# Kernel optimization log

Hardware: AMD Instinct MI355X
Metric: run time of the kernel (lower is better)

The kernel has to match this reference:

```python
import jax, jax.numpy as jnp
import numpy as np
from functools import partial

M = 48          # state dim m (= n in this module)
N = 48          # obs dim n == m
B = 32          # batch of independent trajectories
T = 128         # time steps (lax.scan)
HQ = M * M      # GRU_Q hidden
HSIG = M * M    # GRU_Sigma hidden
HS = N * N      # GRU_S hidden
D_SIG_IN = HQ + M          # GRU_Sigma input
D_S_IN = N * N + 2 * N     # GRU_S input
FC2_IN = HS + HSIG
FC2_HID = FC2_IN
FC2_OUT = N * N


def _lin(k, dout, din):
    kw, kb = jax.random.split(k)
    s = 1.0 / np.sqrt(din)
    W = jax.random.uniform(kw, (dout, din), jnp.float32, -s, s)
    b = jax.random.uniform(kb, (dout,), jnp.float32, -s, s)
    return W, b


def _gru_params(k, din, dh):
    k1, k2, k3, k4 = jax.random.split(k, 4)
    s = 1.0 / np.sqrt(dh)
    Wi = jax.random.uniform(k1, (3 * dh, din), jnp.float32, -s, s)
    Wh = jax.random.uniform(k2, (3 * dh, dh), jnp.float32, -s, s)
    bi = jax.random.uniform(k3, (3 * dh,), jnp.float32, -s, s)
    bh = jax.random.uniform(k4, (3 * dh,), jnp.float32, -s, s)
    return Wi, Wh, bi, bh


def setup_inputs() -> dict:
    key = jax.random.key(0)
    ks = list(jax.random.split(key, 24))
    it = iter(ks)
    inp = {}
    inp['y_seq'] = jax.random.normal(next(it), (T, B, N), jnp.float32)
    inp['x0'] = jax.random.normal(next(it), (B, M), jnp.float32)
    inp['hQ0'] = jax.random.normal(next(it), (B, HQ), jnp.float32)
    inp['hSig0'] = jax.random.normal(next(it), (B, HSIG), jnp.float32)
    inp['hS0'] = jax.random.normal(next(it), (B, HS), jnp.float32)
    # system matrices (f_function surrogate F, observation H)
    inp['F'] = jax.random.normal(next(it), (M, M), jnp.float32) / np.sqrt(M)
    inp['H'] = jax.random.normal(next(it), (N, M), jnp.float32) / np.sqrt(M)
    # GRUs
    inp['WiQ'], inp['WhQ'], inp['biQ'], inp['bhQ'] = _gru_params(next(it), M, HQ)
    inp['WiSig'], inp['WhSig'], inp['biSig'], inp['bhSig'] = _gru_params(next(it), D_SIG_IN, HSIG)
    inp['WiS'], inp['WhS'], inp['biS'], inp['bhS'] = _gru_params(next(it), D_S_IN, HS)
    # FC blocks
    inp['W1'], inp['b1'] = _lin(next(it), N * N, HSIG)
    inp['W2a'], inp['b2a'] = _lin(next(it), FC2_HID, FC2_IN)
    inp['W2b'], inp['b2b'] = _lin(next(it), FC2_OUT, FC2_HID)
    inp['W3'], inp['b3'] = _lin(next(it), M * M, HS + FC2_OUT)
    inp['W4'], inp['b4'] = _lin(next(it), HSIG, HSIG + M * M)
    inp['W5'], inp['b5'] = _lin(next(it), M, M)
    inp['W6'], inp['b6'] = _lin(next(it), M, M)
    inp['W7'], inp['b7'] = _lin(next(it), 2 * N, 2 * N)
    return inp


def _gru_cell(x, h, Wi, Wh, bi, bh):
    # PyTorch GRU cell: r,z,n gate order
    gi = x @ Wi.T + bi
    gh = h @ Wh.T + bh
    ir, iz, inn = jnp.split(gi, 3, axis=-1)
    hr, hz, hn = jnp.split(gh, 3, axis=-1)
    r = jax.nn.sigmoid(ir + hr)
    z = jax.nn.sigmoid(iz + hz)
    ng = jnp.tanh(inn + r * hn)
    return (1.0 - z) * ng + z * h


def _l2norm(x):
    # torch F.normalize(p=2, eps=1e-12)
    return x / jnp.maximum(jnp.linalg.norm(x, axis=-1, keepdims=True), 1e-12)


def reference(y_seq, x0, hQ0, hSig0, hS0, F, H,
              WiQ, WhQ, biQ, bhQ, WiSig, WhSig, biSig, bhSig,
              WiS, WhS, biS, bhS,
              W1, b1, W2a, b2a, W2b, b2b, W3, b3, W4, b4,
              W5, b5, W6, b6, W7, b7):
    relu = jax.nn.relu

    def step(carry, y):
        x_post, x_post_prev, x_prior_prev, y_prev, hQ, hSig, hS = carry
        # step_prior (Lorenz branch): m1x_prior = F(x) @ x ; m1y = H @ m1x_prior
        x_prior = x_post @ F.T                       # [B, M]
        m1y = x_prior @ H.T                          # [B, N]
        # step_KGain_est: four normalized difference features
        obs_diff = _l2norm(y - y_prev)
        obs_innov = _l2norm(y - m1y)
        fw_evol = _l2norm(x_post - x_post_prev)
        fw_upd = _l2norm(x_post - x_prior_prev)
        # KGain_step
        o5 = relu(fw_evol @ W5.T + b5)
        hQ_n = _gru_cell(o5, hQ, WiQ, WhQ, biQ, bhQ)
        o6 = relu(fw_upd @ W6.T + b6)
        hSig_n = _gru_cell(jnp.concatenate([hQ_n, o6], -1), hSig, WiSig, WhSig, biSig, bhSig)
        o1 = relu(hSig_n @ W1.T + b1)
        o7 = relu(jnp.concatenate([obs_diff, obs_innov], -1) @ W7.T + b7)
        hS_n = _gru_cell(jnp.concatenate([o1, o7], -1), hS, WiS, WhS, biS, bhS)
        o2 = relu(jnp.concatenate([hSig_n, hS_n], -1) @ W2a.T + b2a) @ W2b.T + b2b
        o3 = relu(jnp.concatenate([hS_n, o2], -1) @ W3.T + b3)
        o4 = relu(jnp.concatenate([hSig_n, o3], -1) @ W4.T + b4)
        # self.h_Sigma = out_FC4 (GRU_Sigma state overwritten)
        KG = o2.reshape(-1, M, M)                    # KGain, d == m == n
        dy = y - m1y
        x_new = x_prior + jnp.einsum('bij,bj->bi', KG, dy)
        return (x_new, x_post, x_prior, y, hQ_n, o4, hS_n), x_new

    y_prev0 = x0 @ H.T
    carry0 = (x0, x0, x0, y_prev0, hQ0, hSig0, hS0)
    _, x_out = jax.lax.scan(step, carry0, y_seq)     # [T, B, M]
    return x_out
```

## Files before the change

### kernel.cpp

```cpp
#include <hip/hip_runtime.h>


typedef unsigned short u16;
typedef unsigned int u32;
typedef unsigned long long u64;
typedef __attribute__((ext_vector_type(8))) short short8;
typedef __attribute__((ext_vector_type(4))) float f32x4;

#define NBLK 288
#define NLEAF 8
#define LEAFSZ (NBLK / NLEAF)

__device__ __forceinline__ u16 f2bf(float f) {
  union { float f; u32 u; } v; v.f = f;
  u32 r = v.u + 0x7fffu + ((v.u >> 16) & 1u);
  return (u16)(r >> 16);
}

__device__ __forceinline__ float gload_f(const float* p) {
  return __hip_atomic_load(p, __ATOMIC_RELAXED, __HIP_MEMORY_SCOPE_AGENT);
}
__device__ __forceinline__ void gstore_f(float* p, float v) {
  __hip_atomic_store(p, v, __ATOMIC_RELAXED, __HIP_MEMORY_SCOPE_AGENT);
}
__device__ __forceinline__ void gstore_bf(u16* p, u16 v) {
  asm volatile("global_store_short %0, %1, off sc0 sc1"
               :: "v"(p), "v"((u32)v) : "memory");
}
__device__ __forceinline__ short8 gload_frag(const u16* p) {
  u64 lo = __hip_atomic_load((const u64*)p,       __ATOMIC_RELAXED, __HIP_MEMORY_SCOPE_AGENT);
  u64 hi = __hip_atomic_load((const u64*)(p + 4), __ATOMIC_RELAXED, __HIP_MEMORY_SCOPE_AGENT);
  union { u64 q[2]; short8 v; } u; u.q[0] = lo; u.q[1] = hi; return u.v;
}

struct PJob { const float* src; u16* dst; int rows, cols; };
struct PJobs { PJob j[3]; };

__global__ void __launch_bounds__(256) pre_cvt(PJobs jobs) {
  PJob jb = jobs.j[blockIdx.y];
  int r = blockIdx.x;
  if (r >= jb.rows) return;
  const float* s = jb.src + (long)r * jb.cols;
  u16* d = jb.dst + (long)r * jb.cols;
  for (int c = threadIdx.x; c < jb.cols; c += blockDim.x) d[c] = f2bf(s[c]);
}

__global__ void __launch_bounds__(256) sw_cvt(const float* src, u16* dst,
    int cols_in, int col_off, int cols_take, int nkt, int u_row0, int u_dst0) {
  int ul = blockIdx.x;
  int u_row = u_row0 + ul;
  long dstbase = (long)(u_dst0 + ul) * nkt * 512;
  for (int i = threadIdx.x; i < nkt * 64; i += blockDim.x) {
    int kt = i >> 6, l = i & 63;
    int r = u_row * 16 + (l & 15);
    int c = kt * 32 + ((l >> 4) << 3);
    const float* s = src + (long)r * cols_in + col_off + c;
    u16 o[8];
#pragma unroll
    for (int j = 0; j < 8; ++j)
      o[j] = (c + j < cols_take) ? f2bf(s[j]) : (u16)0;
    *(ulonglong2*)(dst + dstbase + (long)kt * 512 + l * 8) = *(ulonglong2*)o;
  }
}

__global__ void __launch_bounds__(256) flat_cp(const u16* src, u16* dst, long n8) {
  long i = (long)blockIdx.x * blockDim.x + threadIdx.x;
  long stride = (long)gridDim.x * blockDim.x;
  for (; i < n8; i += stride)
    ((ulonglong2*)dst)[i] = ((const ulonglong2*)src)[i];
}

struct KParams {
  const float *y_seq, *x0, *hQ0, *hSig0, *hS0, *F, *H;
  const float *biQ, *bhQ, *biSig, *bhSig, *biS, *bhS;
  const float *b1, *b2a, *b2b, *b3, *b4, *W5, *b5, *W6, *b6, *W7, *b7;
  const u16 *WiQp, *WhQp, *WiSigH, *WiSigO, *WhSigp, *WiSp, *WhSp;
  const u16 *W1p, *W2ap, *W2bp, *W3p, *W4p;
  u16 *hQbf, *hSigN, *hSigC, *hSbf, *o1, *o2a, *o2, *o3, *o6, *o7;
  float *ghSig, *ghS, *hQf, *hSigCf, *hSf, *o2f, *xprior, *dy;
  float *out;
  u32 *bar;
};

__device__ __forceinline__ void gridbar(u32* bar) {
  __syncthreads();
  if (threadIdx.x == 0) {
    u32* leaf = bar + (blockIdx.x & (NLEAF - 1)) * 32;
    u32* root = bar + 256;
    u32* gen  = bar + 288;
    u32 g = __hip_atomic_load(gen, __ATOMIC_RELAXED, __HIP_MEMORY_SCOPE_AGENT);
    bool released = false;
    u32 a = __hip_atomic_fetch_add(leaf, 1u, __ATOMIC_RELAXED, __HIP_MEMORY_SCOPE_AGENT);
    if (a == LEAFSZ - 1) {
      __hip_atomic_store(leaf, 0u, __ATOMIC_RELAXED, __HIP_MEMORY_SCOPE_AGENT);
      asm volatile("s_waitcnt vmcnt(0)" ::: "memory");
      u32 r = __hip_atomic_fetch_add(root, 1u, __ATOMIC_RELAXED, __HIP_MEMORY_SCOPE_AGENT);
      if (r == NLEAF - 1) {
        __hip_atomic_store(root, 0u, __ATOMIC_RELAXED, __HIP_MEMORY_SCOPE_AGENT);
        asm volatile("s_waitcnt vmcnt(0)" ::: "memory");
        __hip_atomic_store(gen, g + 1u, __ATOMIC_RELAXED, __HIP_MEMORY_SCOPE_AGENT);
        released = true;
      }
    }
    if (!released) {
      while (__hip_atomic_load(gen, __ATOMIC_RELAXED, __HIP_MEMORY_SCOPE_AGENT) == g) {
        __builtin_amdgcn_s_sleep(2);
      }
    }
  }
  __syncthreads();
}

template<int NCH, bool AG>
__device__ __forceinline__ void mm6(f32x4& acc, const u16* __restrict__ wp,
                                    const u16* __restrict__ ap) {
  short8 aw[2][6], ab[2][6];
#pragma unroll
  for (int i = 0; i < 6; ++i) {
    aw[0][i] = *(const short8*)(wp + (long)i * 512);
    ab[0][i] = AG ? gload_frag(ap + i * 32) : *(const short8*)(ap + i * 32);
  }
#pragma unroll
  for (int ch = 0; ch < NCH; ++ch) {
    const int cur = ch & 1;
    if (ch + 1 < NCH) {
#pragma unroll
      for (int i = 0; i < 6; ++i) {
        aw[cur ^ 1][i] = *(const short8*)(wp + (long)((ch + 1) * 6 + i) * 512);
        ab[cur ^ 1][i] = AG ? gload_frag(ap + ((ch + 1) * 6 + i) * 32)
                            : *(const short8*)(ap + ((ch + 1) * 6 + i) * 32);
      }
    }
#pragma unroll
    for (int i = 0; i < 6; ++i)
      acc = __builtin_amdgcn_mfma_f32_16x16x32_bf16(aw[cur][i], ab[cur][i], acc, 0, 0, 0);
  }
}

__device__ __forceinline__ const u16* wfrag(const u16* Wf, long unit, int NKT, int kt) {
  return Wf + ((long)unit * NKT + kt) * 512;
}

template<bool AG>
__device__ __forceinline__ void mm72(f32x4& acc, const u16* Wf, long unit, int NKT,
                                     int wkt0, const u16* act ,
                                     int astride, int wave, int lane) {
  int k0 = wave * 18;
  const u16* wp = wfrag(Wf, unit, NKT, wkt0 + k0) + lane * 8;
  const u16* ap = act + (long)(lane & 15) * astride + ((lane >> 4) << 3) + k0 * 32;
  mm6<3, AG>(acc, wp, ap);
}

template<bool AG>
__device__ __forceinline__ void mm144(f32x4& acc, const u16* Wf, long unit, int NKT,
                                      const u16* act, int astride, int wave, int lane) {
  int k0 = wave * 36;
  const u16* wp = wfrag(Wf, unit, NKT, k0) + lane * 8;
  const u16* ap = act + (long)(lane & 15) * astride + ((lane >> 4) << 3) + k0 * 32;
  mm6<6, AG>(acc, wp, ap);
}

template<bool AG>
__device__ __forceinline__ void mm_small(f32x4& acc, const u16* Wf, long unit, int NKT,
                                         const u16* act, int astride, int n,
                                         int wave, int lane) {
  if (wave < n) {
    const u16* wp = wfrag(Wf, unit, NKT, wave) + lane * 8;
    const u16* ap = act + (long)(lane & 15) * astride + ((lane >> 4) << 3) + wave * 32;
    short8 a = *(const short8*)wp;
    short8 b = AG ? gload_frag(ap) : *(const short8*)ap;
    acc = __builtin_amdgcn_mfma_f32_16x16x32_bf16(a, b, acc, 0, 0, 0);
  }
}

__device__ __forceinline__ void block_reduce(float* red, const f32x4* acc, int na,
                                             int wave, int lane, float* out) {
  for (int a = 0; a < na; ++a)
    for (int r = 0; r < 4; ++r)
      red[((wave * 4 + a) * 4 + r) * 64 + lane] = acc[a][r];
  __syncthreads();
  for (int a = 0; a < na; ++a) {
    float s = 0.f;
    for (int w = 0; w < 4; ++w) s += red[((w * 4 + a) * 4 + wave) * 64 + lane];
    out[a] = s;
  }
}

__device__ __forceinline__ void fc_unit(float* red, const u16* W, int NKT, int ctl, int hfl,
    const u16* a0, int s0stride, const u16* a1, int s1stride,
    const float* bias, bool do_relu, u16* outbf, float* outf, bool coh_outf,
    int ostride, int wave, int lane) {
  f32x4 acc = {};
  mm72<true>(acc, W, ctl, NKT, 0, a0 + (long)hfl * 16 * s0stride, s0stride, wave, lane);
  if (a1) mm72<true>(acc, W, ctl, NKT, 72, a1 + (long)hfl * 16 * s1stride, s1stride, wave, lane);
  float v;
  block_reduce(red, &acc, 1, wave, lane, &v);
  int c = ctl * 16 + ((lane >> 4) << 2) + wave;
  int b = hfl * 16 + (lane & 15);
  v += bias[c];
  if (do_relu) v = fmaxf(v, 0.f);
  gstore_bf(outbf + (long)b * ostride + c, f2bf(v));
  if (outf) {
    if (coh_outf) gstore_f(outf + (long)b * ostride + c, v);
    else          outf[(long)b * ostride + c] = v;
  }
  __syncthreads();
}

__device__ __forceinline__ void fc144_unit(float* red, const u16* W, int ctl, int hfl,
    const u16* a0, int s0stride, const float* bias, u16* outbf, float* outf, int ostride,
    int wave, int lane) {
  f32x4 acc = {};
  mm144<true>(acc, W, ctl, 144, a0 + (long)hfl * 16 * s0stride, s0stride, wave, lane);
  float v;
  block_reduce(red, &acc, 1, wave, lane, &v);
  int c = ctl * 16 + ((lane >> 4) << 2) + wave;
  int b = hfl * 16 + (lane & 15);
  v += bias[c];
  gstore_bf(outbf + (long)b * ostride + c, f2bf(v));
  if (outf) gstore_f(outf + (long)b * ostride + c, v);
  __syncthreads();
}

__device__ __forceinline__ void gh_unit(float* red, const u16* Wh, const u16* actbf,
                                        const float* bh, float* ghout,
                                        int ctl, int hfl, int wave, int lane) {
  f32x4 acc[3] = {};
  const u16* ah = actbf + (long)hfl * 16 * 2304;
  for (int g = 0; g < 3; ++g)
    mm72<true>(acc[g], Wh, g * 144 + ctl, 72, 0, ah, 2304, wave, lane);
  float v[3];
  block_reduce(red, acc, 3, wave, lane, v);
  int c = ctl * 16 + ((lane >> 4) << 2) + wave;
  int b = hfl * 16 + (lane & 15);
  for (int g = 0; g < 3; ++g)
    ghout[((long)b * 3 + g) * 2304 + c] = v[g] + bh[g * 2304 + c];
  __syncthreads();
}

__device__ __forceinline__ void gru_gi_unit(float* red,
    const u16* WiMain, int NKTm, const u16* a0, int s0s,
    const u16* WiTail, int NKTt, int tailUnitMul, int wkt0t,
    const u16* a1, int s1s, int ntail,
    const float* bi, const float* gh, const float* hold,
    u16* hbf, float* hf32, int ctl, int hfl, int wave, int lane) {
  f32x4 acc[3] = {};
  const u16* ah = a0 + (long)hfl * 16 * s0s;
  const u16* at = a1 + (long)hfl * 16 * s1s;
  for (int g = 0; g < 3; ++g) {
    mm72<true>(acc[g], WiMain, g * 144 + ctl, NKTm, 0, ah, s0s, wave, lane);
    if (ntail == 0) continue;
    if (tailUnitMul) {
      if (wave < ntail) {
        const u16* wp = wfrag(WiMain, g * 144 + ctl, NKTm, wkt0t + wave) + lane * 8;
        short8 a = *(const short8*)wp;
        short8 b = gload_frag(at + (long)(lane & 15) * s1s + ((lane >> 4) << 3) + wave * 32);
        acc[g] = __builtin_amdgcn_mfma_f32_16x16x32_bf16(a, b, acc[g], 0, 0, 0);
      }
    } else {
      mm_small<true>(acc[g], WiTail, g * 144 + ctl, NKTt, at, s1s, ntail, wave, lane);
    }
  }
  float v[3];
  block_reduce(red, acc, 3, wave, lane, v);
  int c = ctl * 16 + ((lane >> 4) << 2) + wave;
  int b = hfl * 16 + (lane & 15);
  float gr = gh[((long)b * 3 + 0) * 2304 + c];
  float gz = gh[((long)b * 3 + 1) * 2304 + c];
  float gn = gh[((long)b * 3 + 2) * 2304 + c];
  float r  = 1.f / (1.f + expf(-(v[0] + bi[c] + gr)));
  float z  = 1.f / (1.f + expf(-(v[1] + bi[2304 + c] + gz)));
  float nn = tanhf(v[2] + bi[4608 + c] + r * gn);
  float h  = (1.f - z) * nn + z * hold[(long)b * 2304 + c];
  gstore_bf(hbf + (long)b * 2304 + c, f2bf(h));
  if (hf32) hf32[(long)b * 2304 + c] = h;
  __syncthreads();
}

__global__ void __launch_bounds__(256, 2) knet_main(KParams p) {
  const int tid  = threadIdx.x;
  const int blk  = blockIdx.x;
  const int lane = tid & 63;
  const int wave = tid >> 6;
  const int ctb  = blk >> 1;
  const int hfb  = blk & 1;

  __shared__ __align__(16) float red[4096];
  __shared__ __align__(16) float sA[1536];
  __shared__ __align__(16) float sB[1536];
  __shared__ __align__(16) float sC[1536];
  __shared__ __align__(16) u16 sO5[2048];
  __shared__ float sN1[32], sN2[32], sN3[32];

  for (int t = 0; t < 128; ++t) {
    const float* y      = p.y_seq + t * 1536;
    const float* xpost  = (t >= 1) ? (p.out + (t - 1) * 1536) : p.x0;
    const float* xpost2 = (t >= 2) ? (p.out + (t - 2) * 1536) : p.x0;
    const u16* hQbf_r = p.hQbf + (t & 1) * (32 * 2304);
    u16* hQbf_w       = p.hQbf + ((t + 1) & 1) * (32 * 2304);
    const float* hQf_r   = (t == 0) ? p.hQ0   : p.hQf;
    const float* hSigf_r = (t == 0) ? p.hSig0 : p.hSigCf;
    const float* hSf_r   = (t == 0) ? p.hS0   : p.hSf;
    float* xpr_w         = p.xprior + (t & 1) * 1536;
    const float* xprprev = p.xprior + ((t + 1) & 1) * 1536;

    if (blk == 0) {
      if (t >= 1) {
        const float* yp = p.y_seq + (t - 1) * 1536;
        for (int i = tid; i < 1536; i += 256) sA[i] = y[i] - yp[i];
      } else {
        for (int i = tid; i < 1536; i += 256) {
          int b = i / 48, j = i - b * 48;
          float s = 0.f;
          for (int k = 0; k < 48; ++k) s += p.x0[b * 48 + k] * p.H[j * 48 + k];
          sA[i] = y[i] - s;
        }
      }
      for (int i = tid; i < 1536; i += 256) {
        int b = i / 48, j = i - b * 48;
        float s = 0.f;
        for (int k = 0; k < 48; ++k) s += gload_f(&xpost[b * 48 + k]) * p.F[j * 48 + k];
        sB[i] = s;
        gstore_f(&xpr_w[i], s);
      }
      __syncthreads();
      for (int i = tid; i < 1536; i += 256) {
        int b = i / 48, j = i - b * 48;
        float s = 0.f;
        for (int k = 0; k < 48; ++k) s += sB[b * 48 + k] * p.H[j * 48 + k];
        s = y[i] - s;
        sC[i] = s;
        gstore_f(&p.dy[i], s);
      }
      __syncthreads();
      if (tid < 32) {
        float s = 0.f;
        for (int k = 0; k < 48; ++k) { float d = sA[tid * 48 + k]; s += d * d; }
        sN1[tid] = 1.f / fmaxf(sqrtf(s), 1e-12f);
      } else if (tid < 64) {
        int b = tid - 32; float s = 0.f;
        for (int k = 0; k < 48; ++k) { float d = sC[b * 48 + k]; s += d * d; }
        sN2[b] = 1.f / fmaxf(sqrtf(s), 1e-12f);
      }
      __syncthreads();
      {
        const float* xpp = (t == 0) ? p.x0 : xprprev;
        for (int i = tid; i < 1536; i += 256)
          sB[i] = gload_f(&xpost[i]) - gload_f(&xpp[i]);
      }
      __syncthreads();
      if (tid < 32) {
        float s = 0.f;
        for (int k = 0; k < 48; ++k) { float d = sB[tid * 48 + k]; s += d * d; }
        sN3[tid] = 1.f / fmaxf(sqrtf(s), 1e-12f);
      }
      __syncthreads();
      for (int i = tid; i < 2048; i += 256) {
        int b = i >> 6, c = i & 63;
        float v = 0.f;
        if (c < 48) {
          v = p.b6[c]; float nb = sN3[b];
          for (int k = 0; k < 48; ++k) v += sB[b * 48 + k] * nb * p.W6[c * 48 + k];
          v = fmaxf(v, 0.f);
        }
        gstore_bf(&p.o6[i], f2bf(v));
      }
      for (int i = tid; i < 3072; i += 256) {
        int b = i / 96, c = i - b * 96;
        float v = p.b7[c];
        float n1 = sN1[b], n2 = sN2[b];
        for (int k = 0; k < 48; ++k) v += sA[b * 48 + k] * n1 * p.W7[c * 96 + k];
        for (int k = 0; k < 48; ++k) v += sC[b * 48 + k] * n2 * p.W7[c * 96 + 48 + k];
        gstore_bf(&p.o7[i], f2bf(fmaxf(v, 0.f)));
      }
      __syncthreads();
    }

    {
      const int rowbase = hfb * 16;
      for (int i = tid; i < 768; i += 256) {
        int r = i / 48, k = i - r * 48;
        int b = rowbase + r;
        sA[i] = gload_f(&xpost[b * 48 + k]) - gload_f(&xpost2[b * 48 + k]);
      }
      __syncthreads();
      if (tid < 16) {
        float s = 0.f;
        for (int k = 0; k < 48; ++k) { float d = sA[tid * 48 + k]; s += d * d; }
        sN1[tid] = 1.f / fmaxf(sqrtf(s), 1e-12f);
      }
      __syncthreads();
      for (int i = tid; i < 1024; i += 256) {
        int r = i >> 6, c = i & 63;
        float v = 0.f;
        if (c < 48) {
          v = p.b5[c]; float nb = sN1[r];
          for (int k = 0; k < 48; ++k) v += sA[r * 48 + k] * nb * p.W5[c * 48 + k];
          v = fmaxf(v, 0.f);
        }
        sO5[i] = f2bf(v);
      }
      __syncthreads();
    }

    {
      f32x4 acc[4] = {};
      const u16* actH  = hQbf_r + (long)hfb * 16 * 2304;
      const u16* actO5 = (const u16*)sO5;
      for (int g = 0; g < 2; ++g) {
        mm_small<false>(acc[g], p.WiQp, g * 144 + ctb, 2, actO5, 64, 2, wave, lane);
        mm72<true>(acc[g], p.WhQp, g * 144 + ctb, 72, 0, actH, 2304, wave, lane);
      }
      mm_small<false>(acc[2], p.WiQp, 2 * 144 + ctb, 2, actO5, 64, 2, wave, lane);
      mm72<true>(acc[3], p.WhQp, 2 * 144 + ctb, 72, 0, actH, 2304, wave, lane);
      float v[4];
      block_reduce(red, acc, 4, wave, lane, v);
      int c = ctb * 16 + ((lane >> 4) << 2) + wave;
      int b = hfb * 16 + (lane & 15);
      float r  = 1.f / (1.f + expf(-(v[0] + p.biQ[c] + p.bhQ[c])));
      float z  = 1.f / (1.f + expf(-(v[1] + p.biQ[2304 + c] + p.bhQ[2304 + c])));
      float nn = tanhf(v[2] + p.biQ[4608 + c] + r * (v[3] + p.bhQ[4608 + c]));
      float h  = (1.f - z) * nn + z * hQf_r[(long)b * 2304 + c];
      p.hQf[(long)b * 2304 + c] = h;
      gstore_bf(hQbf_w + (long)b * 2304 + c, f2bf(h));
      __syncthreads();
    }
    gh_unit(red, p.WhSigp, p.hSigC, p.bhSig, p.ghSig, ctb, hfb, wave, lane);
    gh_unit(red, p.WhSp,   p.hSbf,  p.bhS,   p.ghS,   ctb, hfb, wave, lane);
    gridbar(p.bar);

    gru_gi_unit(red,
                p.WiSigH, 72, hQbf_w, 2304,
                p.WiSigO, 2, 0, 0, p.o6, 64, 2,
                p.biSig, p.ghSig, hSigf_r,
                p.hSigN, nullptr, ctb, hfb, wave, lane);
    gridbar(p.bar);

    fc_unit(red, p.W1p, 72, ctb, hfb,
            p.hSigN, 2304, nullptr, 0,
            p.b1, true, p.o1, nullptr, false, 2304, wave, lane);
    gridbar(p.bar);

    gru_gi_unit(red,
                p.WiSp, 75, p.o1, 2304,
                nullptr, 0, 1, 72, p.o7, 96, 3,
                p.biS, p.ghS, hSf_r,
                p.hSbf, p.hSf, ctb, hfb, wave, lane);
    gridbar(p.bar);

    for (int uu = blk; uu < 576; uu += NBLK) {
      int ctl = uu >> 1, hfl = uu & 1;
      fc_unit(red, p.W2ap, 144, ctl, hfl,
              p.hSigN, 2304, p.hSbf, 2304,
              p.b2a, true, p.o2a, nullptr, false, 4608, wave, lane);
    }
    gridbar(p.bar);

    fc144_unit(red, p.W2bp, ctb, hfb,
               p.o2a, 4608, p.b2b, p.o2, p.o2f, 2304, wave, lane);
    gridbar(p.bar);

    fc_unit(red, p.W3p, 144, ctb, hfb,
            p.hSbf, 2304, p.o2, 2304,
            p.b3, true, p.o3, nullptr, false, 2304, wave, lane);
    if (blk < 32) {
      const int b = blk;
      for (int ii = tid; ii < 48; ii += 256) {
        float s = gload_f(&xpr_w[b * 48 + ii]);
        const float* o2row = p.o2f + (long)b * 2304 + ii * 48;
        const float* dyrow = p.dy + b * 48;
        for (int j = 0; j < 48; ++j) s += gload_f(&o2row[j]) * gload_f(&dyrow[j]);
        gstore_f(&p.out[t * 1536 + b * 48 + ii], s);
      }
    }
    gridbar(p.bar);

    fc_unit(red, p.W4p, 144, ctb, hfb,
            p.hSigN, 2304, p.o3, 2304,
            p.b4, true, p.hSigC, p.hSigCf, false ,
            2304, wave, lane);
    gridbar(p.bar);
  }
}

extern "C" void kernel_launch(void* const* d_in, const int* in_sizes, int n_in,
                              void* d_out, int out_size, void* d_ws, size_t ws_size,
                              hipStream_t stream) {
  if (n_in < 35) return;
  if (in_sizes[0] != 128 * 32 * 48) return;
  if (in_sizes[7] != 6912 * 48) return;
  if (in_sizes[11] != 6912 * 2352) return;
  if (in_sizes[15] != 6912 * 2400) return;
  if (in_sizes[21] != 4608 * 4608) return;
  if (in_sizes[33] != 96 * 96) return;
  if (out_size != 128 * 32 * 48) return;

  float* in[35];
  for (int i = 0; i < 35; ++i) in[i] = (float*)d_in[i];

  char* base = (char*)d_ws;
  size_t used = 0;
  auto alloc = [&](size_t bytes) -> char* {
    char* r = base + used;
    used += (bytes + 255) & ~(size_t)255;
    return r;
  };
  u32* bar      = (u32*)alloc(2048);
  u16* temp     = (u16*)alloc(2304ll * 4608 * 2);
  u16* WiQp     = (u16*)alloc(432ll * 2 * 512 * 2);
  u16* WiSigO   = (u16*)alloc(432ll * 2 * 512 * 2);
  u16* hQbf     = (u16*)alloc(2ll * 32 * 2304 * 2);
  u16* hSigN    = (u16*)alloc(32ll * 2304 * 2);
  u16* hSigC    = (u16*)alloc(32ll * 2304 * 2);
  u16* hSbf     = (u16*)alloc(32ll * 2304 * 2);
  u16* o1b      = (u16*)alloc(32ll * 2304 * 2);
  u16* o2ab     = (u16*)alloc(32ll * 4608 * 2);
  u16* o2b      = (u16*)alloc(32ll * 2304 * 2);
  u16* o3b      = (u16*)alloc(32ll * 2304 * 2);
  u16* o6b      = (u16*)alloc(32ll * 64 * 2);
  u16* o7b      = (u16*)alloc(32ll * 96 * 2);
  float* ghSig  = (float*)alloc(32ll * 6912 * 4);
  float* ghS    = (float*)alloc(32ll * 6912 * 4);
  float* hQf    = (float*)alloc(32ll * 2304 * 4);
  float* hSigCf = (float*)alloc(32ll * 2304 * 4);
  float* hSf    = (float*)alloc(32ll * 2304 * 4);
  float* o2f    = (float*)alloc(32ll * 2304 * 4);
  float* xprior = (float*)alloc(2ll * 1536 * 4);
  float* dy     = (float*)alloc(1536ll * 4);
  if (used > ws_size) return;

  hipMemsetAsync(bar, 0, 2048, stream);

  PJobs pj;
  pj.j[0] = { in[2], hQbf,  32, 2304 };
  pj.j[1] = { in[3], hSigC, 32, 2304 };
  pj.j[2] = { in[4], hSbf,  32, 2304 };
  pre_cvt<<<dim3(32, 3), dim3(256), 0, stream>>>(pj);

  sw_cvt<<<dim3(432), dim3(256), 0, stream>>>(in[7],  WiQp,   48,   0,    48, 2, 0, 0);
  sw_cvt<<<dim3(432), dim3(256), 0, stream>>>(in[11], WiSigO, 2352, 2304, 48, 2, 0, 0);

  struct IP { float* buf; int rows, ci, take, nkt; };
  const IP ips[10] = {
    { in[8],  6912, 2304, 2304, 72 },
    { in[11], 6912, 2352, 2304, 72 },
    { in[12], 6912, 2304, 2304, 72 },
    { in[15], 6912, 2400, 2400, 75 },
    { in[16], 6912, 2304, 2304, 72 },
    { in[19], 2304, 2304, 2304, 72 },
    { in[21], 4608, 4608, 4608, 144 },
    { in[23], 2304, 4608, 4608, 144 },
    { in[25], 2304, 4608, 4608, 144 },
    { in[27], 2304, 4608, 4608, 144 },
  };
  for (int m = 0; m < 10; ++m) {
    int U = ips[m].rows / 16, Uh = U / 2;
    sw_cvt<<<dim3(Uh), dim3(256), 0, stream>>>(ips[m].buf, temp,
        ips[m].ci, 0, ips[m].take, ips[m].nkt, 0, 0);
    sw_cvt<<<dim3(Uh), dim3(256), 0, stream>>>(ips[m].buf, (u16*)ips[m].buf,
        ips[m].ci, 0, ips[m].take, ips[m].nkt, Uh, Uh);
    long n8 = (long)Uh * ips[m].nkt * 64;
    flat_cp<<<dim3(2048), dim3(256), 0, stream>>>(temp, (u16*)ips[m].buf, n8);
  }

  KParams kp;
  kp.y_seq = in[0]; kp.x0 = in[1]; kp.hQ0 = in[2]; kp.hSig0 = in[3]; kp.hS0 = in[4];
  kp.F = in[5]; kp.H = in[6];
  kp.biQ = in[9]; kp.bhQ = in[10];
  kp.biSig = in[13]; kp.bhSig = in[14];
  kp.biS = in[17]; kp.bhS = in[18];
  kp.b1 = in[20]; kp.b2a = in[22]; kp.b2b = in[24]; kp.b3 = in[26]; kp.b4 = in[28];
  kp.W5 = in[29]; kp.b5 = in[30]; kp.W6 = in[31]; kp.b6 = in[32]; kp.W7 = in[33]; kp.b7 = in[34];
  kp.WiQp = WiQp;
  kp.WhQp = (const u16*)in[8];
  kp.WiSigH = (const u16*)in[11];
  kp.WiSigO = WiSigO;
  kp.WhSigp = (const u16*)in[12];
  kp.WiSp = (const u16*)in[15];
  kp.WhSp = (const u16*)in[16];
  kp.W1p = (const u16*)in[19];
  kp.W2ap = (const u16*)in[21];
  kp.W2bp = (const u16*)in[23];
  kp.W3p = (const u16*)in[25];
  kp.W4p = (const u16*)in[27];
  kp.hQbf = hQbf; kp.hSigN = hSigN; kp.hSigC = hSigC; kp.hSbf = hSbf;
  kp.o1 = o1b; kp.o2a = o2ab; kp.o2 = o2b; kp.o3 = o3b; kp.o6 = o6b; kp.o7 = o7b;
  kp.ghSig = ghSig; kp.ghS = ghS; kp.hQf = hQf; kp.hSigCf = hSigCf; kp.hSf = hSf;
  kp.o2f = o2f; kp.xprior = xprior; kp.dy = dy;
  kp.out = (float*)d_out;
  kp.bar = bar;

  knet_main<<<dim3(NBLK), dim3(256), 0, stream>>>(kp);
}
```

Before: 66.48 ms.

## Share activation fragments across gate matrices in multi-output MFMA loops

Adds a mm_multi helper that loads each activation fragment once and reuses it across 2 or 3 weight slices (GRU gates, or the two halves of W2a). The GRU gh, gi and Q gate computations and the FC2a layer now use it instead of separate mm72 calls per gate. FC2a now handles two output tiles per block in one unit rather than looping over 576 units. This cuts redundant coherent global activation loads and adds independent MFMA chains, at the cost of higher register pressure from larger double-buffered fragment arrays.

Measured after the change: 76.47 ms. 1.15x slower.

```diff
diff --git a/kernel.cpp b/kernel.cpp
--- a/kernel.cpp
+++ b/kernel.cpp
@@ -111,6 +111,64 @@
   __syncthreads();
 }
 
+__device__ __forceinline__ const u16* wfrag(const u16* Wf, long unit, int NKT, int kt) {
+  return Wf + ((long)unit * NKT + kt) * 512;
+}
+
+template<int NS, int CHK, int NCH, bool AG>
+__device__ __forceinline__ void mm_multi(f32x4* acc, const u16* __restrict__ wp0,
+                                         long gs, const u16* __restrict__ ap) {
+  short8 aw[2][NS][CHK];
+  short8 ab[2][CHK];
+#pragma unroll
+  for (int i = 0; i < CHK; ++i) {
+    ab[0][i] = AG ? gload_frag(ap + i * 32) : *(const short8*)(ap + i * 32);
+#pragma unroll
+    for (int g = 0; g < NS; ++g)
+      aw[0][g][i] = *(const short8*)(wp0 + (long)g * gs + (long)i * 512);
+  }
+#pragma unroll
+  for (int ch = 0; ch < NCH; ++ch) {
+    const int cur = ch & 1;
+    if (ch + 1 < NCH) {
+#pragma unroll
+      for (int i = 0; i < CHK; ++i) {
+        const int kk = (ch + 1) * CHK + i;
+        ab[cur ^ 1][i] = AG ? gload_frag(ap + kk * 32)
+                            : *(const short8*)(ap + kk * 32);
+#pragma unroll
+        for (int g = 0; g < NS; ++g)
+          aw[cur ^ 1][g][i] = *(const short8*)(wp0 + (long)g * gs + (long)kk * 512);
+      }
+    }
+#pragma unroll
+    for (int i = 0; i < CHK; ++i)
+#pragma unroll
+      for (int g = 0; g < NS; ++g)
+        acc[g] = __builtin_amdgcn_mfma_f32_16x16x32_bf16(aw[cur][g][i], ab[cur][i], acc[g], 0, 0, 0);
+  }
+}
+
+template<bool AG>
+__device__ __forceinline__ void mm72x3(f32x4* acc, const u16* Wf, long unit0, int NKT,
+                                       const u16* act, int astride, int wave, int lane) {
+  int k0 = wave * 18;
+  const u16* wp0 = wfrag(Wf, unit0, NKT, k0) + lane * 8;
+  long gs = 144L * NKT * 512;
+  const u16* ap = act + (long)(lane & 15) * astride + ((lane >> 4) << 3) + k0 * 32;
+  mm_multi<3, 3, 6, AG>(acc, wp0, gs, ap);
+}
+
+__device__ __forceinline__ void mm72x2(f32x4* acc, const u16* Wf, long unit0, int NKT,
+                                       int wkt0, const u16* act, int astride,
+                                       int wave, int lane) {
+  int k0 = wave * 18;
+  const u16* wp0 = wfrag(Wf, unit0, NKT, wkt0 + k0) + lane * 8;
+  long gs = 144L * NKT * 512;
+  const u16* ap = act + (long)(lane & 15) * astride + ((lane >> 4) << 3) + k0 * 32;
+  mm_multi<2, 3, 6, true>(acc, wp0, gs, ap);
+}
+
 template<int NCH, bool AG>
 __device__ __forceinline__ void mm6(f32x4& acc, const u16* __restrict__ wp,
                                     const u16* __restrict__ ap) {
@@ -137,14 +195,10 @@
   }
 }
 
-__device__ __forceinline__ const u16* wfrag(const u16* Wf, long unit, int NKT, int kt) {
-  return Wf + ((long)unit * NKT + kt) * 512;
-}
-
 template<bool AG>
 __device__ __forceinline__ void mm72(f32x4& acc, const u16* Wf, long unit, int NKT,
-                                     int wkt0, const u16* act ,
-                                     int astride, int wave, int lane) {
+                                     int wkt0, const u16* act, int astride,
+                                     int wave, int lane) {
   int k0 = wave * 18;
   const u16* wp = wfrag(Wf, unit, NKT, wkt0 + k0) + lane * 8;
   const u16* ap = act + (long)(lane & 15) * astride + ((lane >> 4) << 3) + k0 * 32;
@@ -207,6 +261,25 @@
   __syncthreads();
 }
 
+__device__ __forceinline__ void fc2_unit(float* red, const u16* W, int ctl, int hfl,
+    const u16* a0, const u16* a1, const float* bias, u16* outbf,
+    int wave, int lane) {
+  f32x4 acc[2] = {};
+  mm72x2(acc, W, ctl, 144, 0,  a0 + (long)hfl * 16 * 2304, 2304, wave, lane);
+  mm72x2(acc, W, ctl, 144, 72, a1 + (long)hfl * 16 * 2304, 2304, wave, lane);
+  float v[2];
+  block_reduce(red, acc, 2, wave, lane, v);
+  int c0 = ctl * 16 + ((lane >> 4) << 2) + wave;
+  int b = hfl * 16 + (lane & 15);
+#pragma unroll
+  for (int s = 0; s < 2; ++s) {
+    int c = c0 + s * 2304;
+    float vv = fmaxf(v[s] + bias[c], 0.f);
+    gstore_bf(outbf + (long)b * 4608 + c, f2bf(vv));
+  }
+  __syncthreads();
+}
+
 __device__ __forceinline__ void fc144_unit(float* red, const u16* W, int ctl, int hfl,
     const u16* a0, int s0stride, const float* bias, u16* outbf, float* outf, int ostride,
     int wave, int lane) {
@@ -227,8 +300,7 @@
                                         int ctl, int hfl, int wave, int lane) {
   f32x4 acc[3] = {};
   const u16* ah = actbf + (long)hfl * 16 * 2304;
-  for (int g = 0; g < 3; ++g)
-    mm72<true>(acc[g], Wh, g * 144 + ctl, 72, 0, ah, 2304, wave, lane);
+  mm72x3<true>(acc, Wh, ctl, 72, ah, 2304, wave, lane);
   float v[3];
   block_reduce(red, acc, 3, wave, lane, v);
   int c = ctl * 16 + ((lane >> 4) << 2) + wave;
@@ -247,18 +319,19 @@
   f32x4 acc[3] = {};
   const u16* ah = a0 + (long)hfl * 16 * s0s;
   const u16* at = a1 + (long)hfl * 16 * s1s;
-  for (int g = 0; g < 3; ++g) {
-    mm72<true>(acc[g], WiMain, g * 144 + ctl, NKTm, 0, ah, s0s, wave, lane);
-    if (ntail == 0) continue;
-    if (tailUnitMul) {
-      if (wave < ntail) {
-        const u16* wp = wfrag(WiMain, g * 144 + ctl, NKTm, wkt0t + wave) + lane * 8;
-        short8 a = *(const short8*)wp;
-        short8 b = gload_frag(at + (long)(lane & 15) * s1s + ((lane >> 4) << 3) + wave * 32);
-        acc[g] = __builtin_amdgcn_mfma_f32_16x16x32_bf16(a, b, acc[g], 0, 0, 0);
-      }
-    } else {
-      mm_small<true>(acc[g], WiTail, g * 144 + ctl, NKTt, at, s1s, ntail, wave, lane);
+  mm72x3<true>(acc, WiMain, ctl, NKTm, ah, s0s, wave, lane);
+  if (ntail) {
+    for (int g = 0; g < 3; ++g) {
+      if (tailUnitMul) {
+        if (wave < ntail) {
+          const u16* wp = wfrag(WiMain, g * 144 + ctl, NKTm, wkt0t + wave) + lane * 8;
+          short8 a = *(const short8*)wp;
+          short8 b = gload_frag(at + (long)(lane & 15) * s1s + ((lane >> 4) << 3) + wave * 32);
+          acc[g] = __builtin_amdgcn_mfma_f32_16x16x32_bf16(a, b, acc[g], 0, 0, 0);
+        }
+      } else {
+        mm_small<true>(acc[g], WiTail, g * 144 + ctl, NKTt, at, s1s, ntail, wave, lane);
+      }
     }
   }
   float v[3];
@@ -407,12 +480,14 @@
       f32x4 acc[4] = {};
       const u16* actH  = hQbf_r + (long)hfb * 16 * 2304;
       const u16* actO5 = (const u16*)sO5;
-      for (int g = 0; g < 2; ++g) {
-        mm_small<false>(acc[g], p.WiQp, g * 144 + ctb, 2, actO5, 64, 2, wave, lane);
-        mm72<true>(acc[g], p.WhQp, g * 144 + ctb, 72, 0, actH, 2304, wave, lane);
-      }
+      mm_small<false>(acc[0], p.WiQp, 0 * 144 + ctb, 2, actO5, 64, 2, wave, lane);
+      mm_small<false>(acc[1], p.WiQp, 1 * 144 + ctb, 2, actO5, 64, 2, wave, lane);
       mm_small<false>(acc[2], p.WiQp, 2 * 144 + ctb, 2, actO5, 64, 2, wave, lane);
-      mm72<true>(acc[3], p.WhQp, 2 * 144 + ctb, 72, 0, actH, 2304, wave, lane);
+      {
+        f32x4 aW[3] = { acc[0], acc[1], acc[3] };
+        mm72x3<true>(aW, p.WhQp, ctb, 72, actH, 2304, wave, lane);
+        acc[0] = aW[0]; acc[1] = aW[1]; acc[3] = aW[2];
+      }
       float v[4];
       block_reduce(red, acc, 4, wave, lane, v);
       int c = ctb * 16 + ((lane >> 4) << 2) + wave;
@@ -448,12 +523,7 @@
                 p.hSbf, p.hSf, ctb, hfb, wave, lane);
     gridbar(p.bar);
 
-    for (int uu = blk; uu < 576; uu += NBLK) {
-      int ctl = uu >> 1, hfl = uu & 1;
-      fc_unit(red, p.W2ap, 144, ctl, hfl,
-              p.hSigN, 2304, p.hSbf, 2304,
-              p.b2a, true, p.o2a, nullptr, false, 4608, wave, lane);
-    }
+    fc2_unit(red, p.W2ap, ctb, hfb, p.hSigN, p.hSbf, p.b2a, p.o2a, wave, lane);
     gridbar(p.bar);
 
     fc144_unit(red, p.W2bp, ctb, hfb,
```
